# Performance work log

Measured on AMD Instinct MI355X. Metric: run time of the kernel, lower is better.

## Reference

```python
import jax, jax.numpy as jnp
import numpy as np
from jax import lax

K = 3          # kernel size
K2 = K * K
STRIDE = 1
PAD = 1
DIL = 1


def _bilinear_sample(x_flat, py, px, H, W):
    """x_flat: [B, C, H*W]; py/px: [B, N] float sampling coords.
    Returns [B, C, N]; zero outside the image (matches DCNv2 CUDA kernel)."""
    y0 = jnp.floor(py)
    x0 = jnp.floor(px)
    dy = py - y0
    dx = px - x0
    y0i = y0.astype(jnp.int32)
    x0i = x0.astype(jnp.int32)

    def gather(yi, xi):
        valid = (yi >= 0) & (yi < H) & (xi >= 0) & (xi < W)
        idx = jnp.clip(yi, 0, H - 1) * W + jnp.clip(xi, 0, W - 1)  # [B, N]
        v = jnp.take_along_axis(x_flat, idx[:, None, :], axis=2)   # [B, C, N]
        return v * valid[:, None, :].astype(x_flat.dtype)

    w00 = ((1 - dy) * (1 - dx))[:, None, :]
    w01 = ((1 - dy) * dx)[:, None, :]
    w10 = (dy * (1 - dx))[:, None, :]
    w11 = (dy * dx)[:, None, :]
    out = gather(y0i, x0i) * w00
    out = out + gather(y0i, x0i + 1) * w01
    out = out + gather(y0i + 1, x0i) * w10
    out = out + gather(y0i + 1, x0i + 1) * w11
    return out


def setup_inputs() -> dict:
    key = jax.random.key(0)
    k1, k2, k3, k4, k5 = jax.random.split(key, 5)
    B, Cin, H, W = 4, 256, 64, 64
    Co = 256
    x = jax.random.normal(k1, (B, Cin, H, W), dtype=jnp.float32)
    # NOTE: original code zero-inits the offset/mask conv; we use small random
    # weights so the bilinear-sampling path is actually exercised.
    w_om = jax.random.normal(k2, (3 * K2, Cin, K, K), dtype=jnp.float32) * 0.01
    b_om = jax.random.normal(k3, (3 * K2,), dtype=jnp.float32) * 0.01
    w_dcn = jax.random.normal(k4, (Co, Cin, K, K), dtype=jnp.float32) * (1.0 / np.sqrt(Cin * K2))
    b_dcn = jax.random.normal(k5, (Co,), dtype=jnp.float32) * 0.01
    return {"x": x, "w_om": w_om, "b_om": b_om, "w_dcn": w_dcn, "b_dcn": b_dcn}


def _forward(x, w_om, b_om, w_dcn, b_dcn):
    B, Cin, H, W = x.shape
    Co = w_dcn.shape[0]
    # offset/mask conv (standard 3x3, pad 1, stride 1)
    om = lax.conv_general_dilated(x, w_om, (STRIDE, STRIDE), [(PAD, PAD), (PAD, PAD)],
                                  rhs_dilation=(DIL, DIL)) + b_om[None, :, None, None]
    Ho, Wo = om.shape[2], om.shape[3]
    o1 = om[:, :K2]            # dy  [B, K2, Ho, Wo]
    o2 = om[:, K2:2 * K2]      # dx
    mask = jax.nn.sigmoid(om[:, 2 * K2:])  # [B, K2, Ho, Wo]

    # base sampling grid: kernel position k = kh*K + kw
    kh = jnp.arange(K2, dtype=jnp.float32) // K
    kw = jnp.arange(K2, dtype=jnp.float32) % K
    base_y = (jnp.arange(Ho, dtype=jnp.float32) * STRIDE - PAD)[None, :] + (kh * DIL)[:, None]  # [K2, Ho]
    base_x = (jnp.arange(Wo, dtype=jnp.float32) * STRIDE - PAD)[None, :] + (kw * DIL)[:, None]  # [K2, Wo]

    py = base_y[None, :, :, None] + o1  # [B, K2, Ho, Wo]
    px = base_x[None, :, None, :] + o2

    N = K2 * Ho * Wo
    x_flat = x.reshape(B, Cin, H * W)
    sampled = _bilinear_sample(x_flat, py.reshape(B, N), px.reshape(B, N), H, W)  # [B, Cin, N]
    sampled = sampled.reshape(B, Cin, K2, Ho * Wo)
    sampled = sampled * mask.reshape(B, 1, K2, Ho * Wo)

    w = w_dcn.reshape(Co, Cin, K2)
    out = jnp.einsum('bckn,ock->bon', sampled, w) + b_dcn[None, :, None]
    out = jax.nn.relu(out)  # only_dcn=False, bn=False -> ReLU
    return out.reshape(B, Co, Ho, Wo)


def reference(x, w_om, b_om, w_dcn, b_dcn):
    return _forward(x, w_om, b_om, w_dcn, b_dcn)
```

## Files before the change

kernel.cpp:

```cpp
#include <hip/hip_runtime.h>
#include <math.h>

typedef _Float16 f16x8 __attribute__((ext_vector_type(8)));
typedef float f32x4 __attribute__((ext_vector_type(4)));
typedef unsigned short ushort_t;

#define HW 4096
#define MFMA16 __builtin_amdgcn_mfma_f32_16x16x32_f16

__device__ __forceinline__ ushort_t f2h_u(float v) {
    union { _Float16 h; ushort_t u; } cv; cv.h = (_Float16)v; return cv.u;
}
__device__ __forceinline__ f16x8 splat8(float v) {
    _Float16 h = (_Float16)v;
    f16x8 r;
    #pragma unroll
    for (int i = 0; i < 8; ++i) r[i] = h;
    return r;
}
__device__ __forceinline__ void bar_lds() {
    asm volatile("s_waitcnt lgkmcnt(0)" ::: "memory");
    __builtin_amdgcn_s_barrier();
}

__global__ __launch_bounds__(256) void prep_w(
    const float* __restrict__ w_dcn, const float* __restrict__ w_om,
    ushort_t* __restrict__ w16, ushort_t* __restrict__ wom16)
{
    int flat = blockIdx.x * 256 + threadIdx.x;
    if (flat < 589824) {
        int kk = flat & 31, co = (flat >> 5) & 255, c8 = (flat >> 13) & 7, k = flat >> 16;
        w16[flat] = f2h_u(w_dcn[(size_t)(co * 256 + c8 * 32 + kk) * 9 + k]);
    } else {
        int o = flat - 589824;
        int kk = o & 31, m = (o >> 5) & 31, c8 = (o >> 10) & 7, k = o >> 13;
        float v = (m < 27) ? w_om[(size_t)(m * 256 + c8 * 32 + kk) * 9 + k] : 0.0f;
        wom16[o] = f2h_u(v);
    }
}

__global__ __launch_bounds__(256) void xpose(
    const float* __restrict__ x, ushort_t* __restrict__ xT)
{
    int b    = blockIdx.x >> 6;
    int pos0 = (blockIdx.x & 63) * 64;
    int tid  = threadIdx.x;
    __shared__ ushort_t lds[64 * 256];

    int posw = tid & 63;
    int ciq  = tid >> 6;
    const float* xb = x + (size_t)b * 256 * HW + pos0 + posw;
    #pragma unroll
    for (int it = 0; it < 8; ++it) {
        int ci = it * 32 + ciq * 8;
        f16x8 hv;
        #pragma unroll
        for (int j = 0; j < 8; ++j)
            hv[j] = (_Float16)xb[(size_t)(ci + j) * HW];
        int off = posw * 512 + ((ci * 2) ^ ((posw & 7) << 4));
        *(f16x8*)((char*)lds + off) = hv;
    }
    __syncthreads();
    int posr = tid >> 2;
    int cg   = tid & 3;
    char* dst = (char*)(xT + ((size_t)(b * HW) + pos0 + posr) * 256);
    #pragma unroll
    for (int u = 0; u < 8; ++u) {
        int cB = u * 64 + cg * 16;
        f16x8 hv = *(const f16x8*)((const char*)lds + posr * 512 + (cB ^ ((posr & 7) << 4)));
        *(f16x8*)(dst + cB) = hv;
    }
}

__global__ __launch_bounds__(256) void om_gemm(
    const ushort_t* __restrict__ xT, const ushort_t* __restrict__ wom16,
    float* __restrict__ part)
{
    int wid = blockIdx.x * 4 + (threadIdx.x >> 6);
    int s  = wid & 7;
    int ho = (wid >> 3) & 63;
    int b  = wid >> 9;
    int l  = threadIdx.x & 63;
    int kb = l >> 4, c16 = l & 15;

    f32x4 zv = {0.f, 0.f, 0.f, 0.f};
    f32x4 acc[2][4];
    #pragma unroll
    for (int i = 0; i < 2; ++i)
        #pragma unroll
        for (int j = 0; j < 4; ++j) acc[i][j] = zv;
    f16x8 hz;
    #pragma unroll
    for (int j = 0; j < 8; ++j) hz[j] = (_Float16)0.0f;

    const ushort_t* xTb = xT + (size_t)b * HW * 256;

    for (int k9 = 0; k9 < 9; ++k9) {
        int kh = k9 / 3, kw = k9 - kh * 3;
        int y = ho - 1 + kh;
        bool yv = (y >= 0) & (y < 64);
        int yc = min(max(y, 0), 63);
        const ushort_t* wp = wom16 + ((size_t)((k9 * 8 + s) * 32 + c16)) * 32 + kb * 8;
        f16x8 a0 = *(const f16x8*)wp;
        f16x8 a1 = *(const f16x8*)(wp + 512);
        f16x8 bf[4];
        #pragma unroll
        for (int jt = 0; jt < 4; ++jt) {
            int wo = jt * 16 + c16;
            int wox = wo + kw - 1;
            bool v = yv & (wox >= 0) & (wox < 64);
            int woc = min(max(wox, 0), 63);
            const ushort_t* sp = xTb + ((size_t)(yc * 64 + woc)) * 256 + s * 32 + kb * 8;
            f16x8 bv = *(const f16x8*)sp;
            bf[jt] = v ? bv : hz;
        }
        #pragma unroll
        for (int jt = 0; jt < 4; ++jt) {
            acc[0][jt] = MFMA16(a0, bf[jt], acc[0][jt], 0, 0, 0);
            acc[1][jt] = MFMA16(a1, bf[jt], acc[1][jt], 0, 0, 0);
        }
    }
    int pos0 = ho * 64;
    #pragma unroll
    for (int i = 0; i < 2; ++i)
        #pragma unroll
        for (int jt = 0; jt < 4; ++jt)
            #pragma unroll
            for (int r = 0; r < 4; ++r) {
                int m = i * 16 + kb * 4 + r;
                part[((size_t)(b * 8 + s) * 32 + m) * HW + pos0 + jt * 16 + c16] = acc[i][jt][r];
            }
}

__global__ __launch_bounds__(256) void om_reduce(
    const float* __restrict__ part, const float* __restrict__ b_om,
    float* __restrict__ py, float* __restrict__ px, float* __restrict__ msk)
{
    int flat = blockIdx.x * 256 + threadIdx.x;
    int pos = flat & 4095;
    int t = flat >> 12;
    int ch = t % 27;
    int b = t / 27;
    float val = b_om[ch];
    #pragma unroll
    for (int pr = 0; pr < 8; ++pr)
        val += part[((size_t)(b * 8 + pr) * 32 + ch) * HW + pos];
    int ho = pos >> 6, wo = pos & 63;
    if (ch < 9) {
        int kh = ch / 3;
        py[(size_t)(b * 9 + ch) * HW + pos] = (float)(ho - 1 + kh) + val;
    } else if (ch < 18) {
        int k = ch - 9, kw = k % 3;
        px[(size_t)(b * 9 + k) * HW + pos] = (float)(wo - 1 + kw) + val;
    } else {
        int k = ch - 18;
        msk[(size_t)(b * 9 + k) * HW + pos] = 1.0f / (1.0f + expf(-val));
    }
}

__global__ __launch_bounds__(512, 2) void dcn_fused(
    const ushort_t* __restrict__ xT, const ushort_t* __restrict__ w16,
    const float* __restrict__ b_dcn,
    const float* __restrict__ py, const float* __restrict__ px,
    const float* __restrict__ msk, float* __restrict__ out)
{
    int bid  = blockIdx.x;
    int b    = bid >> 6;
    int pos0 = (bid & 63) * 64;
    int tid  = threadIdx.x;
    int w    = tid >> 6, l = tid & 63;
    int kb   = l >> 4, c16 = l & 15;
    int g8   = tid & 7, spos = tid >> 3;

    __shared__ __align__(16) ushort_t sB[2][4096];

    const ushort_t* xTb   = xT + (size_t)b * HW * 256;
    const ushort_t* wbase = w16 + (size_t)(w * 32 + c16) * 32 + kb * 8;

    f32x4 zv = {0.f, 0.f, 0.f, 0.f};
    f32x4 acc[2][4];
    #pragma unroll
    for (int i = 0; i < 2; ++i)
        #pragma unroll
        for (int j = 0; j < 4; ++j) acc[i][j] = zv;

    int o00 = 0, o01 = 0, o10 = 0, o11 = 0;
    float tw00 = 0.f, tw01 = 0.f, tw10 = 0.f, tw11 = 0.f;
    f32x4 wA, wB;
    f16x8 gA00, gA01, gA10, gA11;
    f16x8 gB00, gB01, gB10, gB11;
    f16x8 aA00, aA01, aA10, aA11;
    f16x8 aB00, aB01, aB10, aB11;

#define UPD(K9)                                                               \
    do {                                                                      \
        size_t gidx = (size_t)(b * 9 + (K9)) * HW + pos0 + spos;              \
        float fy = py[gidx], fx = px[gidx], mv = msk[gidx];                   \
        float y0f = floorf(fy), x0f = floorf(fx);                             \
        int y0 = (int)y0f, x0 = (int)x0f;                                     \
        float dy = fy - y0f, dx = fx - x0f;                                   \
        bool vy0 = (y0 >= 0) & (y0 < 64);                                     \
        bool vy1 = (y0 >= -1) & (y0 < 63);                                    \
        bool vx0 = (x0 >= 0) & (x0 < 64);                                     \
        bool vx1 = (x0 >= -1) & (x0 < 63);                                    \
        int y0c = min(max(y0, 0), 63), y1c = min(max(y0 + 1, 0), 63);         \
        int x0c = min(max(x0, 0), 63), x1c = min(max(x0 + 1, 0), 63);         \
        o00 = (y0c * 64 + x0c) * 256; o01 = (y0c * 64 + x1c) * 256;           \
        o10 = (y1c * 64 + x0c) * 256; o11 = (y1c * 64 + x1c) * 256;           \
        tw00 = (vy0 && vx0) ? (1.f - dy) * (1.f - dx) * mv : 0.f;             \
        tw01 = (vy0 && vx1) ? (1.f - dy) * dx * mv : 0.f;                     \
        tw10 = (vy1 && vx0) ? dy * (1.f - dx) * mv : 0.f;                     \
        tw11 = (vy1 && vx1) ? dy * dx * mv : 0.f;                             \
    } while (0)

#define ISS(S, CHUNK)                                                         \
    do {                                                                      \
        int cio = ((CHUNK) & 3) * 64 + g8 * 8;                                \
        g##S##00 = *(const f16x8*)(xTb + o00 + cio);                          \
        g##S##01 = *(const f16x8*)(xTb + o01 + cio);                          \
        g##S##10 = *(const f16x8*)(xTb + o10 + cio);                          \
        g##S##11 = *(const f16x8*)(xTb + o11 + cio);                          \
        w##S[0] = tw00; w##S[1] = tw01; w##S[2] = tw10; w##S[3] = tw11;       \
    } while (0)

#define CMB(S, CHUNK)                                                         \
    do {                                                                      \
        f16x8 s00 = splat8(w##S[0]), s01 = splat8(w##S[1]);                   \
        f16x8 s10 = splat8(w##S[2]), s11 = splat8(w##S[3]);                   \
        f16x8 res = g##S##00 * s00 + g##S##01 * s01                           \
                  + g##S##10 * s10 + g##S##11 * s11;                          \
        int byo = (g8 * 1024 + spos * 16) ^ (g8 << 4);                        \
        *(f16x8*)((char*)&sB[(CHUNK) & 1][0] + byo) = res;                    \
    } while (0)

#define LOADA(S, IT)                                                          \
    do {                                                                      \
        const ushort_t* ap = wbase + (size_t)(IT) * 16384;                    \
        a##S##00 = *(const f16x8*)ap;                                         \
        a##S##01 = *(const f16x8*)(ap + 512);                                 \
        a##S##10 = *(const f16x8*)(ap + 8192);                                \
        a##S##11 = *(const f16x8*)(ap + 8192 + 512);                          \
    } while (0)

#define MFMACORE(IT, S)                                                       \
    do {                                                                      \
        const char* bb = (const char*)&sB[(IT) & 1][0];                       \
        f16x8 b0[4], b1[4];                                                   \
        _Pragma("unroll")                                                     \
        for (int jt = 0; jt < 4; ++jt) {                                      \
            int p16 = (jt * 16 + c16) * 16;                                   \
            b0[jt] = *(const f16x8*)(bb + ((kb * 1024 + p16) ^ (kb << 4)));   \
            b1[jt] = *(const f16x8*)(bb + (((kb + 4) * 1024 + p16) ^ ((kb + 4) << 4))); \
        }                                                                     \
        _Pragma("unroll")                                                     \
        for (int jt = 0; jt < 4; ++jt) {                                      \
            acc[0][jt] = MFMA16(a##S##00, b0[jt], acc[0][jt], 0, 0, 0);       \
            acc[1][jt] = MFMA16(a##S##01, b0[jt], acc[1][jt], 0, 0, 0);       \
        }                                                                     \
        _Pragma("unroll")                                                     \
        for (int jt = 0; jt < 4; ++jt) {                                      \
            acc[0][jt] = MFMA16(a##S##10, b1[jt], acc[0][jt], 0, 0, 0);       \
            acc[1][jt] = MFMA16(a##S##11, b1[jt], acc[1][jt], 0, 0, 0);       \
        }                                                                     \
    } while (0)

    UPD(0);
    ISS(A, 0);
    ISS(B, 1);
    LOADA(A, 0);
    CMB(A, 0);
    bar_lds();

    for (int base = 0; base < 34; base += 2) {
        LOADA(B, base + 1);
        if (((base + 2) & 3) == 0) UPD((base + 2) >> 2);
        ISS(A, base + 2);
        CMB(B, base + 1);
        MFMACORE(base, A);
        bar_lds();
        LOADA(A, base + 2);
        ISS(B, base + 3);
        CMB(A, base + 2);
        MFMACORE(base + 1, B);
        bar_lds();
    }
    LOADA(B, 35);
    CMB(B, 35);
    MFMACORE(34, A);
    bar_lds();
    MFMACORE(35, B);

#undef UPD
#undef ISS
#undef CMB
#undef LOADA
#undef MFMACORE

    #pragma unroll
    for (int i = 0; i < 2; ++i)
        #pragma unroll
        for (int r = 0; r < 4; ++r) {
            int co = w * 32 + i * 16 + kb * 4 + r;
            float bias = b_dcn[co];
            float* orow = out + (size_t)(b * 256 + co) * HW + pos0;
            #pragma unroll
            for (int jt = 0; jt < 4; ++jt)
                orow[jt * 16 + c16] = fmaxf(acc[i][jt][r] + bias, 0.f);
        }
}

extern "C" void kernel_launch(void* const* d_in, const int* in_sizes, int n_in,
                              void* d_out, int out_size, void* d_ws, size_t ws_size,
                              hipStream_t stream) {
    const float* x     = (const float*)d_in[0];
    const float* w_om  = (const float*)d_in[1];
    const float* b_om  = (const float*)d_in[2];
    const float* w_dcn = (const float*)d_in[3];
    const float* b_dcn = (const float*)d_in[4];
    float* out = (float*)d_out;

    float* ws = (float*)d_ws;
    float* py   = ws;
    float* px   = ws + 147456;
    float* msk  = ws + 294912;
    ushort_t* w16   = (ushort_t*)(ws + 442368);
    ushort_t* wom16 = (ushort_t*)(ws + 737280);
    ushort_t* xT    = (ushort_t*)(ws + 774144);
    float* part = ws + 2871296;

    prep_w   <<<2592, 256, 0, stream>>>(w_dcn, w_om, w16, wom16);
    xpose    <<<256,  256, 0, stream>>>(x, xT);
    om_gemm  <<<512,  256, 0, stream>>>(xT, wom16, part);
    om_reduce<<<1728, 256, 0, stream>>>(part, b_om, py, px, msk);
    dcn_fused<<<256,  512, 0, stream>>>(xT, w16, b_dcn, py, px, msk, out);
}
```

Measured before the change: 68.93 us.

## Fuse prep kernels, merge offset GEMM with reduction, split DCN K-loop across block halves

Three changes go in together. The weight conversion and input transpose now run in one launch. The offset/mask conv partials are reduced in LDS inside the GEMM kernel, which removes the global partial buffer and a separate reduce launch. The main DCN kernel now uses 1024-thread blocks in which two halves each process half of the 36 K-chunks, then combine their accumulators through LDS before the bias+ReLU epilogue. This cuts launch overhead and global traffic and doubles the waves per block on only 256 blocks, at the cost of larger LDS use and an extra cross-half reduction.

```diff
diff --git a/kernel.cpp b/kernel.cpp
--- a/kernel.cpp
+++ b/kernel.cpp
@@ -23,30 +23,30 @@
     __builtin_amdgcn_s_barrier();
 }
 
-__global__ __launch_bounds__(256) void prep_w(
-    const float* __restrict__ w_dcn, const float* __restrict__ w_om,
-    ushort_t* __restrict__ w16, ushort_t* __restrict__ wom16)
+__global__ __launch_bounds__(256) void prep(
+    const float* __restrict__ x, const float* __restrict__ w_dcn,
+    const float* __restrict__ w_om,
+    ushort_t* __restrict__ w16, ushort_t* __restrict__ wom16,
+    ushort_t* __restrict__ xT)
 {
-    int flat = blockIdx.x * 256 + threadIdx.x;
-    if (flat < 589824) {
-        int kk = flat & 31, co = (flat >> 5) & 255, c8 = (flat >> 13) & 7, k = flat >> 16;
-        w16[flat] = f2h_u(w_dcn[(size_t)(co * 256 + c8 * 32 + kk) * 9 + k]);
-    } else {
-        int o = flat - 589824;
-        int kk = o & 31, m = (o >> 5) & 31, c8 = (o >> 10) & 7, k = o >> 13;
-        float v = (m < 27) ? w_om[(size_t)(m * 256 + c8 * 32 + kk) * 9 + k] : 0.0f;
-        wom16[o] = f2h_u(v);
-    }
-}
-
-__global__ __launch_bounds__(256) void xpose(
-    const float* __restrict__ x, ushort_t* __restrict__ xT)
-{
-    int b    = blockIdx.x >> 6;
-    int pos0 = (blockIdx.x & 63) * 64;
-    int tid  = threadIdx.x;
     __shared__ ushort_t lds[64 * 256];
-
+    int tid = threadIdx.x;
+    if (blockIdx.x < 2592) {
+        int flat = blockIdx.x * 256 + tid;
+        if (flat < 589824) {
+            int kk = flat & 31, co = (flat >> 5) & 255, c8 = (flat >> 13) & 7, k = flat >> 16;
+            w16[flat] = f2h_u(w_dcn[(size_t)(co * 256 + c8 * 32 + kk) * 9 + k]);
+        } else {
+            int o = flat - 589824;
+            int kk = o & 31, m = (o >> 5) & 31, c8 = (o >> 10) & 7, k = o >> 13;
+            float v = (m < 27) ? w_om[(size_t)(m * 256 + c8 * 32 + kk) * 9 + k] : 0.0f;
+            wom16[o] = f2h_u(v);
+        }
+        return;
+    }
+    int xb_id = blockIdx.x - 2592;
+    int b    = xb_id >> 6;
+    int pos0 = (xb_id & 63) * 64;
     int posw = tid & 63;
     int ciq  = tid >> 6;
     const float* xb = x + (size_t)b * 256 * HW + pos0 + posw;
@@ -72,16 +72,20 @@
     }
 }
 
-__global__ __launch_bounds__(256) void om_gemm(
+__global__ __launch_bounds__(512) void om_fused(
     const ushort_t* __restrict__ xT, const ushort_t* __restrict__ wom16,
-    float* __restrict__ part)
+    const float* __restrict__ b_om,
+    float* __restrict__ py, float* __restrict__ px, float* __restrict__ msk)
 {
-    int wid = blockIdx.x * 4 + (threadIdx.x >> 6);
-    int s  = wid & 7;
-    int ho = (wid >> 3) & 63;
-    int b  = wid >> 9;
-    int l  = threadIdx.x & 63;
+    int bid = blockIdx.x;
+    int b  = bid >> 6;
+    int ho = bid & 63;
+    int tid = threadIdx.x;
+    int s  = tid >> 6;
+    int l  = tid & 63;
     int kb = l >> 4, c16 = l & 15;
+
+    __shared__ float sOm[8][2048];
 
     f32x4 zv = {0.f, 0.f, 0.f, 0.f};
     f32x4 acc[2][4];
@@ -106,8 +110,7 @@
         f16x8 bf[4];
         #pragma unroll
         for (int jt = 0; jt < 4; ++jt) {
-            int wo = jt * 16 + c16;
-            int wox = wo + kw - 1;
+            int wox = jt * 16 + c16 + kw - 1;
             bool v = yv & (wox >= 0) & (wox < 64);
             int woc = min(max(wox, 0), 63);
             const ushort_t* sp = xTb + ((size_t)(yc * 64 + woc)) * 256 + s * 32 + kb * 8;
@@ -120,45 +123,48 @@
             acc[1][jt] = MFMA16(a1, bf[jt], acc[1][jt], 0, 0, 0);
         }
     }
-    int pos0 = ho * 64;
     #pragma unroll
     for (int i = 0; i < 2; ++i)
         #pragma unroll
         for (int jt = 0; jt < 4; ++jt)
             #pragma unroll
-            for (int r = 0; r < 4; ++r) {
-                int m = i * 16 + kb * 4 + r;
-                part[((size_t)(b * 8 + s) * 32 + m) * HW + pos0 + jt * 16 + c16] = acc[i][jt][r];
-            }
-}
-
-__global__ __launch_bounds__(256) void om_reduce(
-    const float* __restrict__ part, const float* __restrict__ b_om,
-    float* __restrict__ py, float* __restrict__ px, float* __restrict__ msk)
-{
-    int flat = blockIdx.x * 256 + threadIdx.x;
-    int pos = flat & 4095;
-    int t = flat >> 12;
-    int ch = t % 27;
-    int b = t / 27;
-    float val = b_om[ch];
-    #pragma unroll
-    for (int pr = 0; pr < 8; ++pr)
-        val += part[((size_t)(b * 8 + pr) * 32 + ch) * HW + pos];
-    int ho = pos >> 6, wo = pos & 63;
-    if (ch < 9) {
-        int kh = ch / 3;
-        py[(size_t)(b * 9 + ch) * HW + pos] = (float)(ho - 1 + kh) + val;
-    } else if (ch < 18) {
-        int k = ch - 9, kw = k % 3;
-        px[(size_t)(b * 9 + k) * HW + pos] = (float)(wo - 1 + kw) + val;
-    } else {
-        int k = ch - 18;
-        msk[(size_t)(b * 9 + k) * HW + pos] = 1.0f / (1.0f + expf(-val));
-    }
-}
-
-__global__ __launch_bounds__(512, 2) void dcn_fused(
+            for (int r = 0; r < 4; ++r)
+                sOm[s][(i * 16 + kb * 4 + r) * 64 + jt * 16 + c16] = acc[i][jt][r];
+    __syncthreads();
+
+    int e0 = tid * 4;
+    int m  = e0 >> 6;
+    int pl = e0 & 63;
+    if (m < 27) {
+        f32x4 v = zv;
+        #pragma unroll
+        for (int w8 = 0; w8 < 8; ++w8)
+            v += *(const f32x4*)&sOm[w8][e0];
+        float bias = b_om[m];
+        int pos = ho * 64 + pl;
+        if (m < 9) {
+            int kh = m / 3;
+            float* o = py + (size_t)(b * 9 + m) * HW + pos;
+            #pragma unroll
+            for (int j = 0; j < 4; ++j)
+                o[j] = (float)(ho - 1 + kh) + v[j] + bias;
+        } else if (m < 18) {
+            int k = m - 9, kw = k % 3;
+            float* o = px + (size_t)(b * 9 + k) * HW + pos;
+            #pragma unroll
+            for (int j = 0; j < 4; ++j)
+                o[j] = (float)(pl + j - 1 + kw) + v[j] + bias;
+        } else {
+            int k = m - 18;
+            float* o = msk + (size_t)(b * 9 + k) * HW + pos;
+            #pragma unroll
+            for (int j = 0; j < 4; ++j)
+                o[j] = 1.0f / (1.0f + expf(-(v[j] + bias)));
+        }
+    }
+}
+
+__global__ __launch_bounds__(1024, 1) void dcn_fused(
     const ushort_t* __restrict__ xT, const ushort_t* __restrict__ w16,
     const float* __restrict__ b_dcn,
     const float* __restrict__ py, const float* __restrict__ px,
@@ -168,11 +174,17 @@
     int b    = bid >> 6;
     int pos0 = (bid & 63) * 64;
     int tid  = threadIdx.x;
-    int w    = tid >> 6, l = tid & 63;
+    int h    = tid >> 9;
+    int t5   = tid & 511;
+    int w    = t5 >> 6, l = t5 & 63;
     int kb   = l >> 4, c16 = l & 15;
-    int g8   = tid & 7, spos = tid >> 3;
-
-    __shared__ __align__(16) ushort_t sB[2][4096];
+    int g8   = t5 & 7, spos = t5 >> 3;
+    int c0   = h * 18;
+
+    __shared__ __align__(16) ushort_t sB2[2][2][4096];
+    __shared__ float sR[512 * 33];
+
+    ushort_t (&sB)[2][4096] = sB2[h];
 
     const ushort_t* xTb   = xT + (size_t)b * HW * 256;
     const ushort_t* wbase = w16 + (size_t)(w * 32 + c16) * 32 + kb * 8;
@@ -264,14 +276,14 @@
         }                                                                     \
     } while (0)
 
-    UPD(0);
-    ISS(A, 0);
-    ISS(B, 1);
-    LOADA(A, 0);
-    CMB(A, 0);
+    UPD(c0 >> 2);
+    ISS(A, c0);
+    ISS(B, c0 + 1);
+    LOADA(A, c0);
+    CMB(A, c0);
     bar_lds();
 
-    for (int base = 0; base < 34; base += 2) {
+    for (int base = c0; base < c0 + 16; base += 2) {
         LOADA(B, base + 1);
         if (((base + 2) & 3) == 0) UPD((base + 2) >> 2);
         ISS(A, base + 2);
@@ -284,11 +296,11 @@
         MFMACORE(base + 1, B);
         bar_lds();
     }
-    LOADA(B, 35);
-    CMB(B, 35);
-    MFMACORE(34, A);
+    LOADA(B, c0 + 17);
+    CMB(B, c0 + 17);
+    MFMACORE(c0 + 16, A);
     bar_lds();
-    MFMACORE(35, B);
+    MFMACORE(c0 + 17, B);
 
 #undef UPD
 #undef ISS
@@ -296,17 +308,37 @@
 #undef LOADA
 #undef MFMACORE
 
-    #pragma unroll
-    for (int i = 0; i < 2; ++i)
-        #pragma unroll
-        for (int r = 0; r < 4; ++r) {
-            int co = w * 32 + i * 16 + kb * 4 + r;
-            float bias = b_dcn[co];
-            float* orow = out + (size_t)(b * 256 + co) * HW + pos0;
+    __syncthreads();
+    if (h == 1) {
+        #pragma unroll
+        for (int i = 0; i < 2; ++i)
             #pragma unroll
             for (int jt = 0; jt < 4; ++jt)
-                orow[jt * 16 + c16] = fmaxf(acc[i][jt][r] + bias, 0.f);
-        }
+                #pragma unroll
+                for (int r = 0; r < 4; ++r)
+                    sR[t5 * 33 + (i * 4 + jt) * 4 + r] = acc[i][jt][r];
+    }
+    __syncthreads();
+    if (h == 0) {
+        #pragma unroll
+        for (int i = 0; i < 2; ++i)
+            #pragma unroll
+            for (int jt = 0; jt < 4; ++jt)
+                #pragma unroll
+                for (int r = 0; r < 4; ++r)
+                    acc[i][jt][r] += sR[t5 * 33 + (i * 4 + jt) * 4 + r];
+        #pragma unroll
+        for (int i = 0; i < 2; ++i)
+            #pragma unroll
+            for (int r = 0; r < 4; ++r) {
+                int co = w * 32 + i * 16 + kb * 4 + r;
+                float bias = b_dcn[co];
+                float* orow = out + (size_t)(b * 256 + co) * HW + pos0;
+                #pragma unroll
+                for (int jt = 0; jt < 4; ++jt)
+                    orow[jt * 16 + c16] = fmaxf(acc[i][jt][r] + bias, 0.f);
+            }
+    }
 }
 
 extern "C" void kernel_launch(void* const* d_in, const int* in_sizes, int n_in,
@@ -326,11 +358,8 @@
     ushort_t* w16   = (ushort_t*)(ws + 442368);
     ushort_t* wom16 = (ushort_t*)(ws + 737280);
     ushort_t* xT    = (ushort_t*)(ws + 774144);
-    float* part = ws + 2871296;
-
-    prep_w   <<<2592, 256, 0, stream>>>(w_dcn, w_om, w16, wom16);
-    xpose    <<<256,  256, 0, stream>>>(x, xT);
-    om_gemm  <<<512,  256, 0, stream>>>(xT, wom16, part);
-    om_reduce<<<1728, 256, 0, stream>>>(part, b_om, py, px, msk);
-    dcn_fused<<<256,  512, 0, stream>>>(xT, w16, b_dcn, py, px, msk, out);
-}
+
+    prep     <<<2848, 256,  0, stream>>>(x, w_dcn, w_om, w16, wom16, xT);
+    om_fused <<<256,  512,  0, stream>>>(xT, wom16, b_om, py, px, msk);
+    dcn_fused<<<256,  1024, 0, stream>>>(xT, w16, b_dcn, py, px, msk, out);
+}
```

Measured after the change: 59.94 us, median of 3. 13.0% less time.
